# Kernel tuning notes

Measured on AMD Instinct MI355X. Metric: run time of the kernel, lower is better.

## Reference

```python
import jax, jax.numpy as jnp
import numpy as np

D_MODEL = 1024
NUM_HEADS = 16
HEAD_DIM = D_MODEL // NUM_HEADS


def setup_inputs() -> dict:
    key = jax.random.key(0)
    ks = jax.random.split(key, 11)
    B, S, D = 2, 2048, D_MODEL
    scale = 1.0 / np.sqrt(D)
    inp = {
        "query": jax.random.normal(ks[0], (B, S, D), jnp.float32),
        "key": jax.random.normal(ks[1], (B, S, D), jnp.float32),
        "value": jax.random.normal(ks[2], (B, S, D), jnp.float32),
        "Wq": jax.random.normal(ks[3], (D, D), jnp.float32) * scale,
        "bq": jnp.zeros((D,), jnp.float32),
        "Wk": jax.random.normal(ks[4], (D, D), jnp.float32) * scale,
        "bk": jnp.zeros((D,), jnp.float32),
        "Wv": jax.random.normal(ks[5], (D, D), jnp.float32) * scale,
        "bv": jnp.zeros((D,), jnp.float32),
        "Wo": jax.random.normal(ks[6], (D, D), jnp.float32) * scale,
        "bo": jnp.zeros((D,), jnp.float32),
    }
    return inp


def reference(query, key, value, Wq, bq, Wk, bk, Wv, bv, Wo, bo):
    B, S, D = query.shape
    H, hd = NUM_HEADS, HEAD_DIM
    # linear projections (x @ W^T + b, torch nn.Linear convention)
    Q = query @ Wq.T + bq
    K = key @ Wk.T + bk
    V = value @ Wv.T + bv
    # split heads: [B, S, H, hd] -> [B, H, S, hd]
    Q = Q.reshape(B, S, H, hd).transpose(0, 2, 1, 3)
    K = K.reshape(B, S, H, hd).transpose(0, 2, 1, 3)
    V = V.reshape(B, S, H, hd).transpose(0, 2, 1, 3)
    # scaled dot-product attention (explicit, non-flash)
    scores = jnp.einsum("bhqd,bhkd->bhqk", Q, K) / jnp.sqrt(jnp.float32(hd)).astype(Q.dtype)
    attn = jax.nn.softmax(scores, axis=-1)
    out = jnp.einsum("bhqk,bhkd->bhqd", attn, V)
    # merge heads: [B, H, S, hd] -> [B, S, D]
    out = out.transpose(0, 2, 1, 3).reshape(B, S, D)
    return out @ Wo.T + bo
```

## Files before the change

kernel.cpp:

```cpp
#include <hip/hip_runtime.h>
#include <hip/hip_bf16.h>


constexpr int D_MODEL = 1024;
constexpr int S_LEN   = 2048;
constexpr int BATCH   = 2;
constexpr int NH      = 16;
constexpr int HD      = 64;
constexpr int ROWS    = BATCH * S_LEN;

typedef __attribute__((ext_vector_type(8))) short short8;
typedef __attribute__((ext_vector_type(4))) float float4a;

static __device__ __forceinline__ unsigned short f2bf(float f) {
  union { float f; unsigned u; } v{f};
  unsigned r = v.u + 0x7FFFu + ((v.u >> 16) & 1u);
  return (unsigned short)(r >> 16);
}

static __device__ __forceinline__ unsigned pack_bf16(float a, float b) {
#if __has_builtin(__builtin_amdgcn_cvt_pk_bf16_f32)
  typedef __attribute__((ext_vector_type(2))) __bf16 bf16x2;
  union { bf16x2 v; unsigned u; } c;
  c.v = __builtin_amdgcn_cvt_pk_bf16_f32(a, b);
  return c.u;
#else
  return (unsigned)f2bf(a) | ((unsigned)f2bf(b) << 16);
#endif
}

static __device__ __forceinline__ float bf2f(unsigned short u) {
  union { unsigned u; float f; } v;
  v.u = (unsigned)u << 16;
  return v.f;
}

static __device__ __forceinline__ void async16(const void* g, void* l) {
  __builtin_amdgcn_global_load_lds(
      (const __attribute__((address_space(1))) unsigned int*)g,
      (__attribute__((address_space(3))) unsigned int*)l, 16, 0, 0);
}

struct ConvArgs { const float* s[7]; unsigned short* d[7]; int n[7]; };

__global__ __launch_bounds__(256) void convert_bf16(ConvArgs a) {
  const int which = blockIdx.y;
  const int i = (blockIdx.x * 256 + threadIdx.x) * 8;
  if (i >= a.n[which]) return;
  const float4* s = (const float4*)(a.s[which] + i);
  float4 x = s[0], y = s[1];
  unsigned t[4] = {pack_bf16(x.x, x.y), pack_bf16(x.z, x.w),
                   pack_bf16(y.x, y.y), pack_bf16(y.z, y.w)};
  *(short8*)(a.d[which] + i) = *(short8*)t;
}

template <int MODE>
static __device__ __forceinline__ void gemm_body(
    const unsigned short* __restrict__ A, const unsigned short* __restrict__ W,
    const float* __restrict__ bias, void* __restrict__ Yv, float scale,
    unsigned short* As, unsigned short* Bs, unsigned short* Tb) {
  const int tid = threadIdx.x;
  const int w = tid >> 6, lane = tid & 63;
  const int l15 = lane & 15, quad = lane >> 4;
  const int row0 = blockIdx.x * 128, col0 = blockIdx.y * 128;
  const int wm = (w & 1) * 64, wn = (w >> 1) * 64;

  float4a acc[4][4];
#pragma unroll
  for (int i = 0; i < 4; i++)
#pragma unroll
    for (int j = 0; j < 4; j++) acc[i][j] = (float4a){0.f, 0.f, 0.f, 0.f};

  const int swA = (quad + (wm >> 1) + (l15 >> 1)) & 3;
  const int swB = (quad + (wn >> 1) + (l15 >> 1)) & 3;

  for (int kt = 0; kt < D_MODEL; kt += 32) {
    __syncthreads();
#pragma unroll
    for (int j = 0; j < 2; j++) {
      const int i = w * 2 + j;
      const int r = i * 16 + (lane >> 2);
      const int c = ((lane & 3) - (r >> 1)) & 3;
      async16(W + (size_t)(col0 + r) * D_MODEL + kt + c * 8, (char*)Bs + i * 1024);
      async16(A + (size_t)(row0 + r) * D_MODEL + kt + c * 8, (char*)As + i * 1024);
    }
    __syncthreads();

    short8 af[4], bf[4];
#pragma unroll
    for (int mt = 0; mt < 4; mt++) {
      const int r = wm + mt * 16 + l15;
      af[mt] = *(const short8*)&As[(r * 4 + swA) * 8];
    }
#pragma unroll
    for (int nt = 0; nt < 4; nt++) {
      const int r = wn + nt * 16 + l15;
      bf[nt] = *(const short8*)&Bs[(r * 4 + swB) * 8];
    }
#pragma unroll
    for (int mt = 0; mt < 4; mt++)
#pragma unroll
      for (int nt = 0; nt < 4; nt++)
        acc[mt][nt] = __builtin_amdgcn_mfma_f32_16x16x32_bf16(af[mt], bf[nt], acc[mt][nt], 0, 0, 0);
  }

  int cols[4];
  float bvs[4];
#pragma unroll
  for (int nt = 0; nt < 4; nt++) {
    cols[nt] = col0 + wn + nt * 16 + l15;
    bvs[nt]  = bias[cols[nt]] * ((MODE == 0) ? scale : 1.0f);
  }

  if constexpr (MODE == 0) {
    unsigned short* Y = (unsigned short*)Yv;
#pragma unroll
    for (int mt = 0; mt < 4; mt++)
#pragma unroll
      for (int r = 0; r < 4; r++) {
        const int m = row0 + wm + mt * 16 + quad * 4 + r;
        const int bb = m >> 11, s = m & 2047;
#pragma unroll
        for (int nt = 0; nt < 4; nt++) {
          const int h = cols[nt] >> 6, d = cols[nt] & 63;
          Y[(((size_t)(bb * NH + h)) * S_LEN + s) * HD + d] =
              f2bf(acc[mt][nt][r] * scale + bvs[nt]);
        }
      }
  } else {
    __syncthreads();
    unsigned short* T = Tb + w * (64 * 32);
    unsigned short* Y = (unsigned short*)Yv;
#pragma unroll
    for (int p = 0; p < 2; p++) {
      if (p) { asm volatile("s_waitcnt lgkmcnt(0)" ::: "memory"); }
#pragma unroll
      for (int mi = 0; mi < 2; mi++) {
        const int mt = 2 * p + mi;
#pragma unroll
        for (int r = 0; r < 4; r++) {
          const int sl = mi * 16 + quad * 4 + r;
          const int cch = sl >> 3;
#pragma unroll
          for (int nt = 0; nt < 4; nt++) {
            const int dl = nt * 16 + l15;
            const int slot = cch ^ (dl & 3);
            T[dl * 32 + slot * 8 + (sl & 7)] = f2bf(acc[mt][nt][r] + bvs[nt]);
          }
        }
      }
      asm volatile("s_waitcnt lgkmcnt(0)" ::: "memory");
#pragma unroll
      for (int j = 0; j < 4; j++) {
        const int cid = j * 64 + lane;
        const int dl = cid >> 2;
        const int c  = cid & 3;
        const int slot = c ^ (dl & 3);
        short8 v = *(const short8*)&T[dl * 32 + slot * 8];
        const int col = col0 + wn + dl;
        const int h = col >> 6, d = col & 63;
        const int m = row0 + wm + p * 32 + c * 8;
        const int bb = m >> 11, s = m & 2047;
        *(short8*)&Y[(((size_t)(bb * NH + h)) * HD + d) * S_LEN + s] = v;
      }
    }
  }
}

__global__ __launch_bounds__(256) void gemm_qkv(
    const unsigned short* xq, const unsigned short* xk, const unsigned short* xv,
    const unsigned short* wq, const unsigned short* wk, const unsigned short* wv,
    const float* bq, const float* bk, const float* bv,
    unsigned short* Q, unsigned short* K, unsigned short* Vt) {
  __shared__ unsigned short smem[2 * 128 * 32];
  unsigned short* As = smem;
  unsigned short* Bs = smem + 128 * 32;
  unsigned short* Tb = smem;
  const int z = blockIdx.z;
  if (z == 0)      gemm_body<0>(xq, wq, bq, Q,  0.125f * 1.44269504f, As, Bs, Tb);
  else if (z == 1) gemm_body<0>(xk, wk, bk, K,  1.0f, As, Bs, Tb);
  else             gemm_body<2>(xv, wv, bv, Vt, 1.0f, As, Bs, Tb);
}

__global__ __launch_bounds__(256) void gemm_o(
    const unsigned short* __restrict__ Op, const float* __restrict__ Lp,
    const unsigned short* __restrict__ wo, const float* __restrict__ bo,
    float* __restrict__ out) {
  __shared__ unsigned short As[64 * 32];
  __shared__ unsigned short Bs[128 * 32];
  const int tid = threadIdx.x;
  const int w = tid >> 6, lane = tid & 63;
  const int l15 = lane & 15, quad = lane >> 4;
  const int row0 = blockIdx.x * 64, col0 = blockIdx.y * 128;
  const int wn = w * 32;

  const int ar = w * 16 + (lane >> 2);
  const int cg = lane & 3;
  const int asl = (cg + (ar >> 1)) & 3;
  const int grow = row0 + ar;
  const unsigned short* P0 = Op + (size_t)grow * D_MODEL + cg * 8;
  const unsigned short* P1 = P0 + (size_t)ROWS * D_MODEL;
  const float* L0 = Lp + (size_t)grow * NH;
  const float* L1 = L0 + (size_t)ROWS * NH;

  float4a acc[4][2];
#pragma unroll
  for (int i = 0; i < 4; i++)
#pragma unroll
    for (int j = 0; j < 2; j++) acc[i][j] = (float4a){0.f, 0.f, 0.f, 0.f};

  const int swA = (quad + (l15 >> 1)) & 3;
  const int swB = (quad + (wn >> 1) + (l15 >> 1)) & 3;

  for (int kt = 0; kt < D_MODEL; kt += 32) {
    const int h = kt >> 6;
    const float rinv = 1.0f / (L0[h] + L1[h]);
    short8 a = *(const short8*)(P0 + kt);
    short8 b = *(const short8*)(P1 + kt);
    unsigned t[4];
#pragma unroll
    for (int i = 0; i < 4; i++) {
      const float v0 = (bf2f((unsigned short)a[2 * i]) + bf2f((unsigned short)b[2 * i])) * rinv;
      const float v1 = (bf2f((unsigned short)a[2 * i + 1]) + bf2f((unsigned short)b[2 * i + 1])) * rinv;
      t[i] = pack_bf16(v0, v1);
    }
    __syncthreads();
    *(short8*)&As[(ar * 4 + asl) * 8] = *(short8*)t;
#pragma unroll
    for (int j = 0; j < 2; j++) {
      const int i = w * 2 + j;
      const int r = i * 16 + (lane >> 2);
      const int c = ((lane & 3) - (r >> 1)) & 3;
      async16(wo + (size_t)(col0 + r) * D_MODEL + kt + c * 8, (char*)Bs + i * 1024);
    }
    __syncthreads();

    short8 af[4], bf[2];
#pragma unroll
    for (int mt = 0; mt < 4; mt++) {
      const int r = mt * 16 + l15;
      af[mt] = *(const short8*)&As[(r * 4 + swA) * 8];
    }
#pragma unroll
    for (int nt = 0; nt < 2; nt++) {
      const int r = wn + nt * 16 + l15;
      bf[nt] = *(const short8*)&Bs[(r * 4 + swB) * 8];
    }
#pragma unroll
    for (int mt = 0; mt < 4; mt++)
#pragma unroll
      for (int nt = 0; nt < 2; nt++)
        acc[mt][nt] = __builtin_amdgcn_mfma_f32_16x16x32_bf16(af[mt], bf[nt], acc[mt][nt], 0, 0, 0);
  }

#pragma unroll
  for (int nt = 0; nt < 2; nt++) {
    const int col = col0 + wn + nt * 16 + l15;
    const float bv = bo[col];
#pragma unroll
    for (int mt = 0; mt < 4; mt++)
#pragma unroll
      for (int r = 0; r < 4; r++) {
        const int m = row0 + mt * 16 + quad * 4 + r;
        out[(size_t)m * D_MODEL + col] = acc[mt][nt][r] + bv;
      }
  }
}

__global__ __launch_bounds__(256) void attn_kernel(
    const unsigned short* __restrict__ Qh, const unsigned short* __restrict__ Kh,
    const unsigned short* __restrict__ Vt, unsigned short* __restrict__ Op,
    float* __restrict__ Lp) {
  const int qb = blockIdx.x;
  const int h  = blockIdx.y;
  const int bb = blockIdx.z >> 1, sp = blockIdx.z & 1;
  const int tid = threadIdx.x;
  const int w = tid >> 6, lane = tid & 63;
  const int l15 = lane & 15, quad = lane >> 4;

  __shared__ unsigned short Ks[64 * 64];
  __shared__ unsigned short Vs[64 * 64];
  __shared__ unsigned short Ps[4][32][72];

  const size_t bh = (size_t)(bb * NH + h);
  const unsigned short* Qp = Qh + bh * S_LEN * HD;
  const unsigned short* Kp = Kh + bh * S_LEN * HD;
  const unsigned short* Vp = Vt + bh * (size_t)HD * S_LEN;

  short8 qf[2][2];
#pragma unroll
  for (int qnt = 0; qnt < 2; qnt++)
#pragma unroll
    for (int c = 0; c < 2; c++)
      qf[qnt][c] = *(const short8*)(Qp + (size_t)(qb * 128 + w * 32 + qnt * 16 + l15) * HD +
                                    c * 32 + quad * 8);

  unsigned short ob[8] = {0x3F80, 0x3F80, 0x3F80, 0x3F80, 0x3F80, 0x3F80, 0x3F80, 0x3F80};
  const short8 ones = *(short8*)ob;

  float4a Oacc[2][4];
#pragma unroll
  for (int a = 0; a < 2; a++)
#pragma unroll
    for (int b = 0; b < 4; b++) Oacc[a][b] = (float4a){0.f, 0.f, 0.f, 0.f};
  float4a Lacc[2] = {(float4a){0.f, 0.f, 0.f, 0.f}, (float4a){0.f, 0.f, 0.f, 0.f}};

  const int sw0 = (quad + l15) & 7;
  const int sw1 = (quad + 4 + l15) & 7;

  for (int kb = sp * 1024; kb < sp * 1024 + 1024; kb += 64) {
    __syncthreads();
#pragma unroll
    for (int j = 0; j < 2; j++) {
      const int i = w * 2 + j;
      const int r = i * 8 + (lane >> 3);
      const int c = ((lane & 7) - r) & 7;
      async16(Kp + (size_t)(kb + r) * HD + c * 8, (char*)Ks + i * 1024);
      async16(Vp + (size_t)r * S_LEN + kb + c * 8, (char*)Vs + i * 1024);
    }
    __syncthreads();

#pragma unroll
    for (int mt = 0; mt < 4; mt++) {
      const int rb = (mt * 16 + l15) * 8;
      short8 a0 = *(const short8*)&Ks[(rb + sw0) * 8];
      short8 a1 = *(const short8*)&Ks[(rb + sw1) * 8];
#pragma unroll
      for (int qnt = 0; qnt < 2; qnt++) {
        float4a s = (float4a){0.f, 0.f, 0.f, 0.f};
        s = __builtin_amdgcn_mfma_f32_16x16x32_bf16(a0, qf[qnt][0], s, 0, 0, 0);
        s = __builtin_amdgcn_mfma_f32_16x16x32_bf16(a1, qf[qnt][1], s, 0, 0, 0);
        uint2 pk;
        pk.x = pack_bf16(__builtin_amdgcn_exp2f(s[0]), __builtin_amdgcn_exp2f(s[1]));
        pk.y = pack_bf16(__builtin_amdgcn_exp2f(s[2]), __builtin_amdgcn_exp2f(s[3]));
        *(uint2*)&Ps[w][qnt * 16 + l15][mt * 16 + quad * 4] = pk;
      }
    }
    asm volatile("s_waitcnt lgkmcnt(0)" ::: "memory");

#pragma unroll
    for (int c = 0; c < 2; c++) {
      short8 pa0 = *(const short8*)&Ps[w][l15][c * 32 + quad * 8];
      short8 pa1 = *(const short8*)&Ps[w][16 + l15][c * 32 + quad * 8];
      Lacc[0] = __builtin_amdgcn_mfma_f32_16x16x32_bf16(pa0, ones, Lacc[0], 0, 0, 0);
      Lacc[1] = __builtin_amdgcn_mfma_f32_16x16x32_bf16(pa1, ones, Lacc[1], 0, 0, 0);
      const int vsw = (c * 4 + quad + l15) & 7;
#pragma unroll
      for (int nt = 0; nt < 4; nt++) {
        short8 vb = *(const short8*)&Vs[((nt * 16 + l15) * 8 + vsw) * 8];
        Oacc[0][nt] = __builtin_amdgcn_mfma_f32_16x16x32_bf16(pa0, vb, Oacc[0][nt], 0, 0, 0);
        Oacc[1][nt] = __builtin_amdgcn_mfma_f32_16x16x32_bf16(pa1, vb, Oacc[1][nt], 0, 0, 0);
      }
    }
  }

  if (l15 == 0) {
#pragma unroll
    for (int qnt = 0; qnt < 2; qnt++)
#pragma unroll
      for (int reg = 0; reg < 4; reg++) {
        const int q = qb * 128 + w * 32 + qnt * 16 + quad * 4 + reg;
        Lp[(size_t)sp * ROWS * NH + ((size_t)bb * S_LEN + q) * NH + h] = Lacc[qnt][reg];
      }
  }

  unsigned short* Ob = Op + (size_t)sp * ROWS * D_MODEL;
#pragma unroll
  for (int qnt = 0; qnt < 2; qnt++) {
#pragma unroll
    for (int reg = 0; reg < 4; reg++) {
      const int q = qb * 128 + w * 32 + qnt * 16 + quad * 4 + reg;
      unsigned short* orow = Ob + ((size_t)bb * S_LEN + q) * D_MODEL + h * HD;
#pragma unroll
      for (int nt = 0; nt < 4; nt++)
        orow[nt * 16 + l15] = f2bf(Oacc[qnt][nt][reg]);
    }
  }
}

extern "C" void kernel_launch(void* const* d_in, const int* in_sizes, int n_in,
                              void* d_out, int out_size, void* d_ws, size_t ws_size,
                              hipStream_t stream) {
  const float* query = (const float*)d_in[0];
  const float* key   = (const float*)d_in[1];
  const float* value = (const float*)d_in[2];
  const float* Wq = (const float*)d_in[3];
  const float* bq = (const float*)d_in[4];
  const float* Wk = (const float*)d_in[5];
  const float* bk = (const float*)d_in[6];
  const float* Wv = (const float*)d_in[7];
  const float* bv = (const float*)d_in[8];
  const float* Wo = (const float*)d_in[9];
  const float* bo = (const float*)d_in[10];
  float* out = (float*)d_out;

  char* ws = (char*)d_ws;
  const size_t MB = 1024 * 1024;
  unsigned short* xq16 = (unsigned short*)(ws + 0 * MB);
  unsigned short* xk16 = (unsigned short*)(ws + 8 * MB);
  unsigned short* xv16 = (unsigned short*)(ws + 16 * MB);
  unsigned short* wq16 = (unsigned short*)(ws + 24 * MB);
  unsigned short* wk16 = (unsigned short*)(ws + 26 * MB);
  unsigned short* wv16 = (unsigned short*)(ws + 28 * MB);
  unsigned short* qbuf  = (unsigned short*)(ws + 32 * MB);
  unsigned short* kbuf  = (unsigned short*)(ws + 40 * MB);
  unsigned short* vtbuf = (unsigned short*)(ws + 48 * MB);
  unsigned short* wo16  = (unsigned short*)(ws + 56 * MB);
  float* Lp = (float*)(ws + 58 * MB);
  unsigned short* Op = (unsigned short*)(ws + 0 * MB);

  ConvArgs ca;
  const int NX = ROWS * D_MODEL, NW = D_MODEL * D_MODEL;
  ca.s[0] = query; ca.d[0] = xq16; ca.n[0] = NX;
  ca.s[1] = key;   ca.d[1] = xk16; ca.n[1] = NX;
  ca.s[2] = value; ca.d[2] = xv16; ca.n[2] = NX;
  ca.s[3] = Wq;    ca.d[3] = wq16; ca.n[3] = NW;
  ca.s[4] = Wk;    ca.d[4] = wk16; ca.n[4] = NW;
  ca.s[5] = Wv;    ca.d[5] = wv16; ca.n[5] = NW;
  ca.s[6] = Wo;    ca.d[6] = wo16; ca.n[6] = NW;
  hipLaunchKernelGGL(convert_bf16, dim3(NX / 2048, 7), dim3(256), 0, stream, ca);

  dim3 gqkv(ROWS / 128, D_MODEL / 128, 3);
  hipLaunchKernelGGL(gemm_qkv, gqkv, dim3(256), 0, stream,
                     xq16, xk16, xv16, wq16, wk16, wv16, bq, bk, bv,
                     qbuf, kbuf, vtbuf);

  dim3 ga(S_LEN / 128, NH, BATCH * 2);
  hipLaunchKernelGGL(attn_kernel, ga, dim3(256), 0, stream, qbuf, kbuf, vtbuf, Op, Lp);

  dim3 go(ROWS / 64, D_MODEL / 128);
  hipLaunchKernelGGL(gemm_o, go, dim3(256), 0, stream, Op, Lp, wo16, bo, out);
}
```

Before: 230.3 us.

## Double-buffer 32-key attention tiles, split keys three ways, remap GEMM blocks

The attention loop now walks 32-key tiles and double-buffers K/V in LDS, prefetching the next tile while it computes the current one, with a single barrier per iteration. The key range is split three ways instead of two, and gemm_o sums the three partial outputs and normalisers. The QKV, attention and output GEMM grids are flattened to 1D with a block index remap meant to group tiles that share data, and the PV MFMAs are wrapped in s_setprio with a launch-bounds occupancy hint. This trades more partial-sum traffic and smaller MFMA batches per barrier for better latency hiding and more parallel work.

New measurement: 264.4 us. 1.15x slower.

```diff
diff --git a/kernel.cpp b/kernel.cpp
--- a/kernel.cpp
+++ b/kernel.cpp
@@ -8,6 +8,7 @@
 constexpr int NH      = 16;
 constexpr int HD      = 64;
 constexpr int ROWS    = BATCH * S_LEN;
+constexpr int NSPLIT  = 3;
 
 typedef __attribute__((ext_vector_type(8))) short short8;
 typedef __attribute__((ext_vector_type(4))) float float4a;
@@ -58,11 +59,11 @@
 static __device__ __forceinline__ void gemm_body(
     const unsigned short* __restrict__ A, const unsigned short* __restrict__ W,
     const float* __restrict__ bias, void* __restrict__ Yv, float scale,
+    int row0, int col0,
     unsigned short* As, unsigned short* Bs, unsigned short* Tb) {
   const int tid = threadIdx.x;
   const int w = tid >> 6, lane = tid & 63;
   const int l15 = lane & 15, quad = lane >> 4;
-  const int row0 = blockIdx.x * 128, col0 = blockIdx.y * 128;
   const int wm = (w & 1) * 64, wn = (w >> 1) * 64;
 
   float4a acc[4][4];
@@ -176,10 +177,15 @@
   unsigned short* As = smem;
   unsigned short* Bs = smem + 128 * 32;
   unsigned short* Tb = smem;
-  const int z = blockIdx.z;
-  if (z == 0)      gemm_body<0>(xq, wq, bq, Q,  0.125f * 1.44269504f, As, Bs, Tb);
-  else if (z == 1) gemm_body<0>(xk, wk, bk, K,  1.0f, As, Bs, Tb);
-  else             gemm_body<2>(xv, wv, bv, Vt, 1.0f, As, Bs, Tb);
+  const int n = blockIdx.x;
+  const int m = n >> 3;
+  const int bx = m & 31;
+  const int g  = (n & 7) + 8 * (m >> 5);
+  const int by = g & 7, z = g >> 3;
+  const int row0 = bx * 128, col0 = by * 128;
+  if (z == 0)      gemm_body<0>(xq, wq, bq, Q,  0.125f * 1.44269504f, row0, col0, As, Bs, Tb);
+  else if (z == 1) gemm_body<0>(xk, wk, bk, K,  1.0f, row0, col0, As, Bs, Tb);
+  else             gemm_body<2>(xv, wv, bv, Vt, 1.0f, row0, col0, As, Bs, Tb);
 }
 
 __global__ __launch_bounds__(256) void gemm_o(
@@ -191,7 +197,9 @@
   const int tid = threadIdx.x;
   const int w = tid >> 6, lane = tid & 63;
   const int l15 = lane & 15, quad = lane >> 4;
-  const int row0 = blockIdx.x * 64, col0 = blockIdx.y * 128;
+  const int n = blockIdx.x;
+  const int by = n & 7, bx = n >> 3;
+  const int row0 = bx * 64, col0 = by * 128;
   const int wn = w * 32;
 
   const int ar = w * 16 + (lane >> 2);
@@ -200,8 +208,10 @@
   const int grow = row0 + ar;
   const unsigned short* P0 = Op + (size_t)grow * D_MODEL + cg * 8;
   const unsigned short* P1 = P0 + (size_t)ROWS * D_MODEL;
+  const unsigned short* P2 = P1 + (size_t)ROWS * D_MODEL;
   const float* L0 = Lp + (size_t)grow * NH;
   const float* L1 = L0 + (size_t)ROWS * NH;
+  const float* L2 = L1 + (size_t)ROWS * NH;
 
   float4a acc[4][2];
 #pragma unroll
@@ -214,14 +224,17 @@
 
   for (int kt = 0; kt < D_MODEL; kt += 32) {
     const int h = kt >> 6;
-    const float rinv = 1.0f / (L0[h] + L1[h]);
+    const float rinv = 1.0f / (L0[h] + L1[h] + L2[h]);
     short8 a = *(const short8*)(P0 + kt);
     short8 b = *(const short8*)(P1 + kt);
+    short8 c = *(const short8*)(P2 + kt);
     unsigned t[4];
 #pragma unroll
     for (int i = 0; i < 4; i++) {
-      const float v0 = (bf2f((unsigned short)a[2 * i]) + bf2f((unsigned short)b[2 * i])) * rinv;
-      const float v1 = (bf2f((unsigned short)a[2 * i + 1]) + bf2f((unsigned short)b[2 * i + 1])) * rinv;
+      const float v0 = (bf2f((unsigned short)a[2 * i]) + bf2f((unsigned short)b[2 * i]) +
+                        bf2f((unsigned short)c[2 * i])) * rinv;
+      const float v1 = (bf2f((unsigned short)a[2 * i + 1]) + bf2f((unsigned short)b[2 * i + 1]) +
+                        bf2f((unsigned short)c[2 * i + 1])) * rinv;
       t[i] = pack_bf16(v0, v1);
     }
     __syncthreads();
@@ -230,8 +243,8 @@
     for (int j = 0; j < 2; j++) {
       const int i = w * 2 + j;
       const int r = i * 16 + (lane >> 2);
-      const int c = ((lane & 3) - (r >> 1)) & 3;
-      async16(wo + (size_t)(col0 + r) * D_MODEL + kt + c * 8, (char*)Bs + i * 1024);
+      const int c2 = ((lane & 3) - (r >> 1)) & 3;
+      async16(wo + (size_t)(col0 + r) * D_MODEL + kt + c2 * 8, (char*)Bs + i * 1024);
     }
     __syncthreads();
 
@@ -267,26 +280,40 @@
   }
 }
 
-__global__ __launch_bounds__(256) void attn_kernel(
+__global__ __launch_bounds__(256, 6) void attn_kernel(
     const unsigned short* __restrict__ Qh, const unsigned short* __restrict__ Kh,
     const unsigned short* __restrict__ Vt, unsigned short* __restrict__ Op,
     float* __restrict__ Lp) {
-  const int qb = blockIdx.x;
-  const int h  = blockIdx.y;
-  const int bb = blockIdx.z >> 1, sp = blockIdx.z & 1;
+  const int n   = blockIdx.x;
+  const int idx = n >> 3;
+  const int qb  = idx & 15;
+  const int g   = (n & 7) + 8 * (idx >> 4);
+  const int h   = g & 15;
+  const int z   = g >> 4;
+  const int bb  = z / NSPLIT, sp = z % NSPLIT;
+
   const int tid = threadIdx.x;
   const int w = tid >> 6, lane = tid & 63;
   const int l15 = lane & 15, quad = lane >> 4;
 
-  __shared__ unsigned short Ks[64 * 64];
-  __shared__ unsigned short Vs[64 * 64];
-  __shared__ unsigned short Ps[4][32][72];
+  __shared__ unsigned short Ks[2][32 * 64];
+  __shared__ unsigned short Vs[2][64 * 32];
+  __shared__ unsigned short Ps[4][32][40];
 
   const size_t bh = (size_t)(bb * NH + h);
   const unsigned short* Qp = Qh + bh * S_LEN * HD;
   const unsigned short* Kp = Kh + bh * S_LEN * HD;
   const unsigned short* Vp = Vt + bh * (size_t)HD * S_LEN;
 
+  const int krow = w * 8 + (lane >> 3);
+  const int kcol = (((lane & 7) - (lane >> 3)) & 7) * 8;
+  const unsigned short* Kg = Kp + (size_t)krow * HD + kcol;
+  const int vrow = w * 16 + (lane >> 2);
+  const int vcol = (((lane & 3) - ((lane >> 2) & 3)) & 3) * 8;
+  const unsigned short* Vg = Vp + (size_t)vrow * S_LEN + vcol;
+  char* Kl = (char*)&Ks[0][0] + (w * 64 + lane) * 16;
+  char* Vl = (char*)&Vs[0][0] + (w * 64 + lane) * 16;
+
   short8 qf[2][2];
 #pragma unroll
   for (int qnt = 0; qnt < 2; qnt++)
@@ -307,24 +334,30 @@
 
   const int sw0 = (quad + l15) & 7;
   const int sw1 = (quad + 4 + l15) & 7;
-
-  for (int kb = sp * 1024; kb < sp * 1024 + 1024; kb += 64) {
-    __syncthreads();
-#pragma unroll
-    for (int j = 0; j < 2; j++) {
-      const int i = w * 2 + j;
-      const int r = i * 8 + (lane >> 3);
-      const int c = ((lane & 7) - r) & 7;
-      async16(Kp + (size_t)(kb + r) * HD + c * 8, (char*)Ks + i * 1024);
-      async16(Vp + (size_t)r * S_LEN + kb + c * 8, (char*)Vs + i * 1024);
-    }
-    __syncthreads();
-
-#pragma unroll
-    for (int mt = 0; mt < 4; mt++) {
+  const int vsw = (quad + l15) & 3;
+
+  const int t0 = (sp * 64) / NSPLIT;
+  const int t1 = ((sp + 1) * 64) / NSPLIT;
+
+  async16(Kg + (size_t)t0 * 32 * HD, Kl);
+  async16(Vg + t0 * 32, Vl);
+  __syncthreads();
+
+  for (int it = t0; it < t1; ++it) {
+    const int cur = (it - t0) & 1;
+    if (it + 1 < t1) {
+      const int nb = cur ^ 1;
+      async16(Kg + (size_t)(it + 1) * 32 * HD, Kl + nb * 4096);
+      async16(Vg + (it + 1) * 32, Vl + nb * 4096);
+    }
+    const unsigned short* Kb = &Ks[cur][0];
+    const unsigned short* Vb = &Vs[cur][0];
+
+#pragma unroll
+    for (int mt = 0; mt < 2; mt++) {
       const int rb = (mt * 16 + l15) * 8;
-      short8 a0 = *(const short8*)&Ks[(rb + sw0) * 8];
-      short8 a1 = *(const short8*)&Ks[(rb + sw1) * 8];
+      short8 a0 = *(const short8*)&Kb[(rb + sw0) * 8];
+      short8 a1 = *(const short8*)&Kb[(rb + sw1) * 8];
 #pragma unroll
       for (int qnt = 0; qnt < 2; qnt++) {
         float4a s = (float4a){0.f, 0.f, 0.f, 0.f};
@@ -338,20 +371,19 @@
     }
     asm volatile("s_waitcnt lgkmcnt(0)" ::: "memory");
 
-#pragma unroll
-    for (int c = 0; c < 2; c++) {
-      short8 pa0 = *(const short8*)&Ps[w][l15][c * 32 + quad * 8];
-      short8 pa1 = *(const short8*)&Ps[w][16 + l15][c * 32 + quad * 8];
-      Lacc[0] = __builtin_amdgcn_mfma_f32_16x16x32_bf16(pa0, ones, Lacc[0], 0, 0, 0);
-      Lacc[1] = __builtin_amdgcn_mfma_f32_16x16x32_bf16(pa1, ones, Lacc[1], 0, 0, 0);
-      const int vsw = (c * 4 + quad + l15) & 7;
-#pragma unroll
-      for (int nt = 0; nt < 4; nt++) {
-        short8 vb = *(const short8*)&Vs[((nt * 16 + l15) * 8 + vsw) * 8];
-        Oacc[0][nt] = __builtin_amdgcn_mfma_f32_16x16x32_bf16(pa0, vb, Oacc[0][nt], 0, 0, 0);
-        Oacc[1][nt] = __builtin_amdgcn_mfma_f32_16x16x32_bf16(pa1, vb, Oacc[1][nt], 0, 0, 0);
-      }
-    }
+    short8 pa0 = *(const short8*)&Ps[w][l15][quad * 8];
+    short8 pa1 = *(const short8*)&Ps[w][16 + l15][quad * 8];
+    __builtin_amdgcn_s_setprio(1);
+    Lacc[0] = __builtin_amdgcn_mfma_f32_16x16x32_bf16(pa0, ones, Lacc[0], 0, 0, 0);
+    Lacc[1] = __builtin_amdgcn_mfma_f32_16x16x32_bf16(pa1, ones, Lacc[1], 0, 0, 0);
+#pragma unroll
+    for (int nt = 0; nt < 4; nt++) {
+      short8 vb = *(const short8*)&Vb[((nt * 16 + l15) * 4 + vsw) * 8];
+      Oacc[0][nt] = __builtin_amdgcn_mfma_f32_16x16x32_bf16(pa0, vb, Oacc[0][nt], 0, 0, 0);
+      Oacc[1][nt] = __builtin_amdgcn_mfma_f32_16x16x32_bf16(pa1, vb, Oacc[1][nt], 0, 0, 0);
+    }
+    __builtin_amdgcn_s_setprio(0);
+    __syncthreads();
   }
 
   if (l15 == 0) {
@@ -420,14 +452,12 @@
   ca.s[6] = Wo;    ca.d[6] = wo16; ca.n[6] = NW;
   hipLaunchKernelGGL(convert_bf16, dim3(NX / 2048, 7), dim3(256), 0, stream, ca);
 
-  dim3 gqkv(ROWS / 128, D_MODEL / 128, 3);
-  hipLaunchKernelGGL(gemm_qkv, gqkv, dim3(256), 0, stream,
+  hipLaunchKernelGGL(gemm_qkv, dim3(768), dim3(256), 0, stream,
                      xq16, xk16, xv16, wq16, wk16, wv16, bq, bk, bv,
                      qbuf, kbuf, vtbuf);
 
-  dim3 ga(S_LEN / 128, NH, BATCH * 2);
-  hipLaunchKernelGGL(attn_kernel, ga, dim3(256), 0, stream, qbuf, kbuf, vtbuf, Op, Lp);
-
-  dim3 go(ROWS / 64, D_MODEL / 128);
-  hipLaunchKernelGGL(gemm_o, go, dim3(256), 0, stream, Op, Lp, wo16, bo, out);
-}
+  hipLaunchKernelGGL(attn_kernel, dim3(16 * 16 * BATCH * NSPLIT), dim3(256), 0, stream,
+                     qbuf, kbuf, vtbuf, Op, Lp);
+
+  hipLaunchKernelGGL(gemm_o, dim3(512), dim3(256), 0, stream, Op, Lp, wo16, bo, out);
+}
```
